# Kernel tuning notes

Measured on AMD Instinct MI355X. Metric: run time of the kernel, lower is better.

The kernel has to match this reference:

```python
import jax, jax.numpy as jnp
import numpy as np

DIM = 512
NUM_HEADS = 8
HEAD_DIM = DIM // NUM_HEADS
EPS = 1e-12  # F.normalize default eps


def _l2norm(x):
    # F.normalize: x / max(||x||_2, eps) along last dim
    n = jnp.sqrt(jnp.sum(x * x, axis=-1, keepdims=True))
    return x / jnp.maximum(n, EPS)


def setup_inputs() -> dict:
    key = jax.random.key(0)
    ks = jax.random.split(key, 7)
    B, N, K = 8, 4096, 256
    scale = 1.0 / np.sqrt(DIM)
    return {
        "X_flat": jax.random.normal(ks[0], (B, N, DIM), jnp.float32),
        "S_tokens": jax.random.normal(ks[1], (B, K, DIM), jnp.float32),
        "Wq": jax.random.normal(ks[2], (DIM, DIM), jnp.float32) * scale,
        "Wk": jax.random.normal(ks[3], (DIM, DIM), jnp.float32) * scale,
        "Wv": jax.random.normal(ks[4], (DIM, DIM), jnp.float32) * scale,
        "Wo": jax.random.normal(ks[5], (DIM, DIM), jnp.float32) * scale,
        "temperature": jnp.ones((NUM_HEADS, 1, 1), jnp.float32),
    }


def reference(X_flat, S_tokens, Wq, Wk, Wv, Wo, temperature):
    B, N, C = X_flat.shape
    K = S_tokens.shape[1]
    H, D = NUM_HEADS, HEAD_DIM
    # torch Linear: y = x @ W.T
    q = (X_flat @ Wq.T).reshape(B, N, H, D).transpose(0, 2, 1, 3)   # (B,H,N,D)
    k = (S_tokens @ Wk.T).reshape(B, K, H, D).transpose(0, 2, 1, 3)  # (B,H,K,D)
    v = (S_tokens @ Wv.T).reshape(B, K, H, D).transpose(0, 2, 1, 3)  # (B,H,K,D)
    q = _l2norm(q)
    k = _l2norm(k)
    attn = jnp.einsum('bhnd,bhkd->bhnk', q, k) * temperature  # temperature (H,1,1) broadcasts
    attn = jax.nn.softmax(attn, axis=-1)
    out = jnp.einsum('bhnk,bhkd->bhnd', attn, v)
    out = out.transpose(0, 2, 1, 3).reshape(B, N, C)
    out = out @ Wo.T
    return X_flat + out
```

## Files before the change

### kernel.cpp

```cpp
#include <hip/hip_runtime.h>
#include <hip/hip_bf16.h>


typedef __bf16 bf16;
typedef __attribute__((ext_vector_type(8))) __bf16 bf16x8;
typedef __attribute__((ext_vector_type(4))) float f32x4;

#if __has_builtin(__builtin_amdgcn_exp2f)
#define EXP2(x) __builtin_amdgcn_exp2f(x)
#else
#define EXP2(x) exp2f(x)
#endif

__device__ __forceinline__ void gload_lds16(const void* g, void* l) {
  __builtin_amdgcn_global_load_lds(
      (__attribute__((address_space(1))) void*)g,
      (__attribute__((address_space(3))) void*)l, 16, 0, 0);
}

__device__ __forceinline__ unsigned pack2(float a, float b) {
  unsigned short x = __builtin_bit_cast(unsigned short, (bf16)a);
  unsigned short y = __builtin_bit_cast(unsigned short, (bf16)b);
  return (unsigned)x | ((unsigned)y << 16);
}

__global__ __launch_bounds__(256) void cvt_all(
    const float* __restrict__ X, const float* __restrict__ S,
    const float* __restrict__ Wq, const float* __restrict__ Wk,
    const float* __restrict__ Wv, const float* __restrict__ Wo,
    bf16* __restrict__ Xb, bf16* __restrict__ Sb, bf16* __restrict__ Wqb,
    bf16* __restrict__ Wkb, bf16* __restrict__ Wvb, bf16* __restrict__ Wob) {
  int i = blockIdx.x * 256 + threadIdx.x;
  const float* src;
  bf16* dst;
  int r;
  if (i < 2097152) {
    src = X; dst = Xb; r = i;
  } else if (i < 2228224) {
    src = S; dst = Sb; r = i - 2097152;
  } else {
    int j = i - 2228224;
    int w = j >> 15;
    r = j & 32767;
    src = (w == 0) ? Wq : (w == 1) ? Wk : (w == 2) ? Wv : Wo;
    dst = (w == 0) ? Wqb : (w == 1) ? Wkb : (w == 2) ? Wvb : Wob;
  }
  float4 a = *(const float4*)(src + (size_t)r * 8);
  float4 b = *(const float4*)(src + (size_t)r * 8 + 4);
  uint4 v;
  v.x = pack2(a.x, a.y);
  v.y = pack2(a.z, a.w);
  v.z = pack2(b.x, b.y);
  v.w = pack2(b.z, b.w);
  *(uint4*)(dst + (size_t)r * 8) = v;
}

__global__ __launch_bounds__(256) void proj_all(
    const bf16* __restrict__ Xb, const bf16* __restrict__ Sb,
    const bf16* __restrict__ Wqb, const bf16* __restrict__ Wkb,
    const bf16* __restrict__ Wvb, const float* __restrict__ temp,
    bf16* __restrict__ Q, bf16* __restrict__ Kn, bf16* __restrict__ Vt) {
  __shared__ __align__(16) char smem[49152];

  const int lg = (blockIdx.x & 7) * 144 + (blockIdx.x >> 3);

  const bf16* A;
  const bf16* W;
  int m0, kind;
  if (lg < 1024) {
    kind = 0; A = Xb; W = Wqb; m0 = (lg >> 2) * 128;
  } else if (lg < 1088) {
    kind = 1; A = Sb; W = Wkb; m0 = ((lg - 1024) >> 2) * 128;
  } else {
    kind = 2; A = Sb; W = Wvb; m0 = ((lg - 1088) >> 2) * 128;
  }
  const int n0 = (lg & 3) * 128;

  const int tid = threadIdx.x;
  const int wid = tid >> 6, lane = tid & 63;
  const int wr = wid >> 1, wc = wid & 1;
  const int g = lane >> 4, c16 = lane & 15;
  const int r0 = tid >> 2, cc0 = tid & 3;
  const int r1 = (256 + tid) >> 2, cc1 = tid & 3;
  const int dst0 = (tid & ~63) * 16, dst1 = (256 + (tid & ~63)) * 16;

  f32x4 acc[4][4] = {};

#define PSTAGE(kb, buf)                                                     \
  {                                                                         \
    char* as = smem + (buf) * 8192;                                         \
    char* bs = smem + 24576 + (buf) * 8192;                                 \
    gload_lds16(A + (size_t)(m0 + r0) * 512 + (kb) + cc0 * 8, as + dst0);   \
    gload_lds16(A + (size_t)(m0 + r1) * 512 + (kb) + cc1 * 8, as + dst1);   \
    gload_lds16(W + (size_t)(n0 + r0) * 512 + (kb) + cc0 * 8, bs + dst0);   \
    gload_lds16(W + (size_t)(n0 + r1) * 512 + (kb) + cc1 * 8, bs + dst1);   \
  }

#define PCOMPUTE(buf)                                                       \
  {                                                                         \
    const bf16* as = (const bf16*)(smem + (buf) * 8192);                    \
    const bf16* bs = (const bf16*)(smem + 24576 + (buf) * 8192);            \
    bf16x8 af[4], bfr[4];                                                   \
    _Pragma("unroll") for (int mi = 0; mi < 4; ++mi) af[mi] =               \
        *(const bf16x8*)(as + (wr * 64 + mi * 16 + c16) * 32 + g * 8);      \
    _Pragma("unroll") for (int ni = 0; ni < 4; ++ni) bfr[ni] =              \
        *(const bf16x8*)(bs + (wc * 64 + ni * 16 + c16) * 32 + g * 8);      \
    _Pragma("unroll") for (int mi = 0; mi < 4; ++mi)                        \
        _Pragma("unroll") for (int ni = 0; ni < 4; ++ni) acc[mi][ni] =      \
            __builtin_amdgcn_mfma_f32_16x16x32_bf16(af[mi], bfr[ni],        \
                                                    acc[mi][ni], 0, 0, 0);  \
  }

  PSTAGE(0, 0);
  PSTAGE(32, 1);
  int bufc = 0;
  for (int t = 0; t < 14; ++t) {
    int bufn = bufc + 2;
    if (bufn >= 3) bufn -= 3;
    PSTAGE((t + 2) * 32, bufn);
    asm volatile("s_waitcnt vmcnt(8)" ::: "memory");
    __builtin_amdgcn_s_barrier();
    PCOMPUTE(bufc);
    __builtin_amdgcn_s_barrier();
    if (++bufc == 3) bufc = 0;
  }
  asm volatile("s_waitcnt vmcnt(4)" ::: "memory");
  __builtin_amdgcn_s_barrier();
  PCOMPUTE(bufc);
  __builtin_amdgcn_s_barrier();
  if (++bufc == 3) bufc = 0;
  asm volatile("s_waitcnt vmcnt(0)" ::: "memory");
  __builtin_amdgcn_s_barrier();
  PCOMPUTE(bufc);

  __syncthreads();

  if (kind != 2) {
    bf16* C = (kind == 0) ? Q : Kn;
    const float sc =
        (kind == 0) ? temp[(n0 + wc * 64) >> 6] * 1.44269504088896f : 1.0f;
    char* eps = smem + wid * 8192;
#pragma unroll
    for (int mi = 0; mi < 4; ++mi) {
      float ss[4];
#pragma unroll
      for (int j = 0; j < 4; ++j) {
        float s = 0.f;
#pragma unroll
        for (int ni = 0; ni < 4; ++ni) {
          float v = acc[mi][ni][j];
          s += v * v;
        }
        ss[j] = s;
      }
#pragma unroll
      for (int msk = 1; msk < 16; msk <<= 1)
#pragma unroll
        for (int j = 0; j < 4; ++j) ss[j] += __shfl_xor(ss[j], msk, 64);
      float inv[4];
#pragma unroll
      for (int j = 0; j < 4; ++j)
        inv[j] = rsqrtf(fmaxf(ss[j], 1e-24f)) * sc;
#pragma unroll
      for (int ni = 0; ni < 4; ++ni)
#pragma unroll
        for (int j = 0; j < 4; ++j) {
          int row = mi * 16 + g * 4 + j, col = ni * 16 + c16;
          int off = (row * 128 + col * 2) ^ ((row & 7) << 4);
          *(bf16*)(eps + off) = (bf16)(acc[mi][ni][j] * inv[j]);
        }
    }
    asm volatile("s_waitcnt lgkmcnt(0)" ::: "memory");
#pragma unroll
    for (int it = 0; it < 8; ++it) {
      int c = it * 64 + lane;
      int row = c >> 3, ch = c & 7;
      int off = (row * 128 + ch * 16) ^ ((row & 7) << 4);
      bf16x8 v = *(const bf16x8*)(eps + off);
      *(bf16x8*)(C + (size_t)(m0 + wr * 64 + row) * 512 + n0 + wc * 64 +
                 ch * 8) = v;
    }
  } else {
#pragma unroll
    for (int mi = 0; mi < 4; ++mi) {
      int m = m0 + wr * 64 + mi * 16 + g * 4;
      int b = m >> 8, tt = m & 255;
#pragma unroll
      for (int ni = 0; ni < 4; ++ni) {
        int col = n0 + wc * 64 + ni * 16 + c16;
        int h = col >> 6, d = col & 63;
        uint2 v;
        v.x = pack2(acc[mi][ni][0], acc[mi][ni][1]);
        v.y = pack2(acc[mi][ni][2], acc[mi][ni][3]);
        *(uint2*)(Vt + ((size_t)((b * 8 + h) * 64 + d) * 256 + tt)) = v;
      }
    }
  }
#undef PSTAGE
#undef PCOMPUTE
}

__global__ __launch_bounds__(256) void out_gemm(
    const bf16* __restrict__ O, const bf16* __restrict__ Wob,
    const float* __restrict__ Xres, float* __restrict__ out) {
  __shared__ __align__(16) char smem[49152];

  const int lg = (blockIdx.x & 7) * 128 + (blockIdx.x >> 3);
  const int m0 = (lg >> 2) * 128, n0 = (lg & 3) * 128;

  const int tid = threadIdx.x;
  const int wid = tid >> 6, lane = tid & 63;
  const int wr = wid >> 1, wc = wid & 1;
  const int g = lane >> 4, c16 = lane & 15;
  const int r0 = tid >> 2, cc0 = tid & 3;
  const int r1 = (256 + tid) >> 2, cc1 = tid & 3;
  const int dst0 = (tid & ~63) * 16, dst1 = (256 + (tid & ~63)) * 16;

  f32x4 acc[4][4] = {};

#define OSTAGE(kb, buf)                                                      \
  {                                                                          \
    char* as = smem + (buf) * 8192;                                          \
    char* bs = smem + 24576 + (buf) * 8192;                                  \
    gload_lds16(O + (size_t)(m0 + r0) * 512 + (kb) + cc0 * 8, as + dst0);    \
    gload_lds16(O + (size_t)(m0 + r1) * 512 + (kb) + cc1 * 8, as + dst1);    \
    gload_lds16(Wob + (size_t)(n0 + r0) * 512 + (kb) + cc0 * 8, bs + dst0);  \
    gload_lds16(Wob + (size_t)(n0 + r1) * 512 + (kb) + cc1 * 8, bs + dst1);  \
  }

#define OCOMPUTE(buf)                                                       \
  {                                                                         \
    const bf16* as = (const bf16*)(smem + (buf) * 8192);                    \
    const bf16* bs = (const bf16*)(smem + 24576 + (buf) * 8192);            \
    bf16x8 af[4], bfr[4];                                                   \
    _Pragma("unroll") for (int mi = 0; mi < 4; ++mi) af[mi] =               \
        *(const bf16x8*)(as + (wr * 64 + mi * 16 + c16) * 32 + g * 8);      \
    _Pragma("unroll") for (int ni = 0; ni < 4; ++ni) bfr[ni] =              \
        *(const bf16x8*)(bs + (wc * 64 + ni * 16 + c16) * 32 + g * 8);      \
    _Pragma("unroll") for (int mi = 0; mi < 4; ++mi)                        \
        _Pragma("unroll") for (int ni = 0; ni < 4; ++ni) acc[mi][ni] =      \
            __builtin_amdgcn_mfma_f32_16x16x32_bf16(af[mi], bfr[ni],        \
                                                    acc[mi][ni], 0, 0, 0);  \
  }

  OSTAGE(0, 0);
  OSTAGE(32, 1);
  int bufc = 0;
  for (int t = 0; t < 14; ++t) {
    int bufn = bufc + 2;
    if (bufn >= 3) bufn -= 3;
    OSTAGE((t + 2) * 32, bufn);
    asm volatile("s_waitcnt vmcnt(8)" ::: "memory");
    __builtin_amdgcn_s_barrier();
    OCOMPUTE(bufc);
    __builtin_amdgcn_s_barrier();
    if (++bufc == 3) bufc = 0;
  }
  asm volatile("s_waitcnt vmcnt(4)" ::: "memory");
  __builtin_amdgcn_s_barrier();
  OCOMPUTE(bufc);
  __builtin_amdgcn_s_barrier();
  if (++bufc == 3) bufc = 0;
  asm volatile("s_waitcnt vmcnt(0)" ::: "memory");
  __builtin_amdgcn_s_barrier();
  OCOMPUTE(bufc);

  __syncthreads();

  char* eps = smem + wid * 8192;
#pragma unroll
  for (int p = 0; p < 2; ++p) {
#pragma unroll
    for (int mm = 0; mm < 2; ++mm)
#pragma unroll
      for (int ni = 0; ni < 4; ++ni)
#pragma unroll
        for (int j = 0; j < 4; ++j) {
          int row = mm * 16 + g * 4 + j, col = ni * 16 + c16;
          int off = (row * 256 + col * 4) ^ ((row & 7) << 4);
          *(float*)(eps + off) = acc[p * 2 + mm][ni][j];
        }
    asm volatile("s_waitcnt lgkmcnt(0)" ::: "memory");
#pragma unroll
    for (int it = 0; it < 8; ++it) {
      int c = it * 64 + lane;
      int row = c >> 4, ch = c & 15;
      int off = (row * 256 + ch * 16) ^ ((row & 7) << 4);
      float4 v = *(const float4*)(eps + off);
      size_t gr = (size_t)(m0 + wr * 64 + p * 32 + row) * 512 + n0 +
                  wc * 64 + ch * 4;
      float4 x = *(const float4*)(Xres + gr);
      v.x += x.x;
      v.y += x.y;
      v.z += x.z;
      v.w += x.w;
      *(float4*)(out + gr) = v;
    }
    asm volatile("s_waitcnt lgkmcnt(0)" ::: "memory");
  }
#undef OSTAGE
#undef OCOMPUTE
}

__global__ __launch_bounds__(256) void attn_fused(
    const bf16* __restrict__ Qn, const bf16* __restrict__ Kn,
    const bf16* __restrict__ Vt, bf16* __restrict__ O) {
  __shared__ __align__(16) char smem[65536];

  const int tid = threadIdx.x;
  const int w = tid >> 6, lane = tid & 63;
  const int g = lane >> 4, c16 = lane & 15;
  const int lg = (blockIdx.x & 7) * 256 + (blockIdx.x >> 3);
  const int nt = lg & 31, h = (lg >> 5) & 7, b = lg >> 8;
  const int n0 = nt * 128;

  {
    const bf16* Ksrc = Kn + ((size_t)b * 256) * 512 + h * 64;
    const bf16* Vsrc = Vt + (size_t)((b * 8 + h) * 64) * 256;
#pragma unroll
    for (int it = 0; it < 8; ++it) {
      int base = it * 256 + w * 64;
      int c = base + lane;
      int ii = c >> 6, rr = c & 63;
      int fc16 = rr >> 2, fg = rr & 3;
      int kmi = ii >> 1, ks_ = ii & 1;
      gload_lds16(Ksrc + (size_t)(kmi * 16 + fc16) * 512 + ks_ * 32 + fg * 8,
                  smem + base * 16);
      int vks = ii >> 2, vni = ii & 3;
      gload_lds16(Vsrc + (size_t)(vni * 16 + fc16) * 256 + vks * 32 + fg * 8,
                  smem + 32768 + base * 16);
    }
  }
  const bf16* Qsrc = Qn + ((size_t)b * 4096 + n0) * 512 + h * 64;
  bf16x8 qf0[2], qf1[2];
  {
    const bf16* q0 = Qsrc + (size_t)(w * 16 + c16) * 512;
    const bf16* q1 = Qsrc + (size_t)(64 + w * 16 + c16) * 512;
    qf0[0] = *(const bf16x8*)(q0 + g * 8);
    qf0[1] = *(const bf16x8*)(q0 + 32 + g * 8);
    qf1[0] = *(const bf16x8*)(q1 + g * 8);
    qf1[1] = *(const bf16x8*)(q1 + 32 + g * 8);
  }
  __syncthreads();

  f32x4 sacc0[16] = {}, sacc1[16] = {};
#pragma unroll
  for (int mi = 0; mi < 16; ++mi) {
#pragma unroll
    for (int s = 0; s < 2; ++s) {
      bf16x8 kf =
          *(const bf16x8*)(smem + ((mi * 2 + s) * 64 + c16 * 4 + g) * 16);
      sacc0[mi] = __builtin_amdgcn_mfma_f32_16x16x32_bf16(kf, qf0[s],
                                                          sacc0[mi], 0, 0, 0);
      sacc1[mi] = __builtin_amdgcn_mfma_f32_16x16x32_bf16(kf, qf1[s],
                                                          sacc1[mi], 0, 0, 0);
    }
  }

  float mxa[4] = {-1e30f, -1e30f, -1e30f, -1e30f};
  float mxb[4] = {-1e30f, -1e30f, -1e30f, -1e30f};
#pragma unroll
  for (int mi = 0; mi < 16; ++mi)
#pragma unroll
    for (int j = 0; j < 4; ++j) {
      mxa[j] = fmaxf(mxa[j], sacc0[mi][j]);
      mxb[j] = fmaxf(mxb[j], sacc1[mi][j]);
    }
  float mx0 = fmaxf(fmaxf(mxa[0], mxa[1]), fmaxf(mxa[2], mxa[3]));
  float mx1 = fmaxf(fmaxf(mxb[0], mxb[1]), fmaxf(mxb[2], mxb[3]));
  mx0 = fmaxf(mx0, __shfl_xor(mx0, 16, 64));
  mx0 = fmaxf(mx0, __shfl_xor(mx0, 32, 64));
  mx1 = fmaxf(mx1, __shfl_xor(mx1, 16, 64));
  mx1 = fmaxf(mx1, __shfl_xor(mx1, 32, 64));
  float sa[4] = {0.f, 0.f, 0.f, 0.f}, sb[4] = {0.f, 0.f, 0.f, 0.f};
#pragma unroll
  for (int mi = 0; mi < 16; ++mi)
#pragma unroll
    for (int j = 0; j < 4; ++j) {
      float p0 = EXP2(sacc0[mi][j] - mx0);
      float p1 = EXP2(sacc1[mi][j] - mx1);
      sacc0[mi][j] = p0;
      sacc1[mi][j] = p1;
      sa[j] += p0;
      sb[j] += p1;
    }
  float sum0 = (sa[0] + sa[1]) + (sa[2] + sa[3]);
  float sum1 = (sb[0] + sb[1]) + (sb[2] + sb[3]);
  sum0 += __shfl_xor(sum0, 16, 64);
  sum0 += __shfl_xor(sum0, 32, 64);
  sum1 += __shfl_xor(sum1, 16, 64);
  sum1 += __shfl_xor(sum1, 32, 64);
  float inv0 = 1.0f / sum0, inv1 = 1.0f / sum1;

  __syncthreads();

  char* pslice = smem + w * 8192;

#define DO_PV(SACC, INV, P)                                                  \
  {                                                                          \
    _Pragma("unroll") for (int mi = 0; mi < 16; ++mi) {                      \
      int cl = (mi >> 1) * 64 + c16 * 4 + ((mi & 1) * 2 + (g >> 1));         \
      uint2 v;                                                               \
      v.x = pack2(SACC[mi][0], SACC[mi][1]);                                 \
      v.y = pack2(SACC[mi][2], SACC[mi][3]);                                 \
      *(uint2*)(pslice + cl * 16 + (g & 1) * 8) = v;                         \
    }                                                                        \
    asm volatile("s_waitcnt lgkmcnt(0)" ::: "memory");                       \
    __builtin_amdgcn_sched_barrier(0);                                       \
    f32x4 oacc[4] = {};                                                      \
    _Pragma("unroll") for (int ks = 0; ks < 8; ++ks) {                       \
      bf16x8 pa =                                                            \
          *(const bf16x8*)(pslice + (ks * 64 + c16 * 4 + g) * 16);           \
      _Pragma("unroll") for (int ni = 0; ni < 4; ++ni) {                     \
        bf16x8 vb = *(const bf16x8*)(                                        \
            smem + 32768 + ((ks * 4 + ni) * 64 + c16 * 4 + g) * 16);         \
        oacc[ni] = __builtin_amdgcn_mfma_f32_16x16x32_bf16(pa, vb,           \
                                                           oacc[ni], 0,0,0); \
      }                                                                      \
    }                                                                        \
    asm volatile("s_waitcnt lgkmcnt(0)" ::: "memory");                       \
    __builtin_amdgcn_sched_barrier(0);                                       \
    _Pragma("unroll") for (int ni = 0; ni < 4; ++ni)                         \
        _Pragma("unroll") for (int j = 0; j < 4; ++j) {                      \
      int row = g * 4 + j, col = ni * 16 + c16;                              \
      int off = (row * 128 + col * 2) ^ ((row & 7) << 4);                    \
      *(bf16*)(pslice + off) = (bf16)(oacc[ni][j] * (INV));                  \
    }                                                                        \
    asm volatile("s_waitcnt lgkmcnt(0)" ::: "memory");                       \
    __builtin_amdgcn_sched_barrier(0);                                       \
    _Pragma("unroll") for (int it = 0; it < 2; ++it) {                       \
      int c = it * 64 + lane;                                                \
      int row = c >> 3, ch = c & 7;                                          \
      int off = (row * 128 + ch * 16) ^ ((row & 7) << 4);                    \
      bf16x8 v = *(const bf16x8*)(pslice + off);                             \
      *(bf16x8*)(O + ((size_t)b * 4096 + n0 + (P) * 64 + w * 16 + row) *     \
                         512 + h * 64 + ch * 8) = v;                         \
    }                                                                        \
    asm volatile("s_waitcnt lgkmcnt(0)" ::: "memory");                       \
    __builtin_amdgcn_sched_barrier(0);                                       \
  }

  DO_PV(sacc0, inv0, 0);
  DO_PV(sacc1, inv1, 1);
#undef DO_PV
}

extern "C" void kernel_launch(void* const* d_in, const int* in_sizes, int n_in,
                              void* d_out, int out_size, void* d_ws,
                              size_t ws_size, hipStream_t stream) {
  const float* X = (const float*)d_in[0];
  const float* S = (const float*)d_in[1];
  const float* Wq = (const float*)d_in[2];
  const float* Wk = (const float*)d_in[3];
  const float* Wv = (const float*)d_in[4];
  const float* Wo = (const float*)d_in[5];
  const float* temp = (const float*)d_in[6];
  float* out = (float*)d_out;

  char* ws = (char*)d_ws;
  bf16* Qws = (bf16*)ws;
  bf16* Kws = (bf16*)(ws + 33554432);
  bf16* Vtws = (bf16*)(ws + 35651584);
  bf16* Wqb = (bf16*)(ws + 37748736);
  bf16* Wkb = (bf16*)(ws + 38273024);
  bf16* Wvb = (bf16*)(ws + 38797312);
  bf16* Wob = (bf16*)(ws + 39321600);

  bf16* Xb = (bf16*)d_out;
  bf16* Sb = (bf16*)((char*)d_out + 33554432);

  cvt_all<<<dim3(9216), dim3(256), 0, stream>>>(X, S, Wq, Wk, Wv, Wo, Xb, Sb,
                                                Wqb, Wkb, Wvb, Wob);
  proj_all<<<dim3(1152), dim3(256), 0, stream>>>(Xb, Sb, Wqb, Wkb, Wvb, temp,
                                                 Qws, Kws, Vtws);
  attn_fused<<<dim3(2048), dim3(256), 0, stream>>>(Qws, Kws, Vtws, Qws);
  out_gemm<<<dim3(1024), dim3(256), 0, stream>>>(Qws, Wob, X, out);
}
```

Before: 148.3 us.

## Store Q/K/V in MFMA-fragment order so attention loads are contiguous

The projection epilogue now writes Q, K and V directly in the per-(batch,head) fragment order that the attention MFMAs consume. Attention can then load K/V into LDS and Q into registers with contiguous per-lane 16-byte accesses instead of strided row gathers. The projection is split into two launches, K/V first and then Q, because Q now reuses the bf16 S buffer region in the output and must be written after S is consumed. This adds a launch and scattered epilogue stores in exchange for simpler, coalesced loads in the attention kernel.

```diff
diff --git a/kernel.cpp b/kernel.cpp
--- a/kernel.cpp
+++ b/kernel.cpp
@@ -55,26 +55,34 @@
   *(uint4*)(dst + (size_t)r * 8) = v;
 }
 
+template <int PHASE>
 __global__ __launch_bounds__(256) void proj_all(
     const bf16* __restrict__ Xb, const bf16* __restrict__ Sb,
     const bf16* __restrict__ Wqb, const bf16* __restrict__ Wkb,
     const bf16* __restrict__ Wvb, const float* __restrict__ temp,
-    bf16* __restrict__ Q, bf16* __restrict__ Kn, bf16* __restrict__ Vt) {
+    bf16* __restrict__ Qf, bf16* __restrict__ Kf, bf16* __restrict__ Vf) {
   __shared__ __align__(16) char smem[49152];
-
-  const int lg = (blockIdx.x & 7) * 144 + (blockIdx.x >> 3);
 
   const bf16* A;
   const bf16* W;
-  int m0, kind;
-  if (lg < 1024) {
-    kind = 0; A = Xb; W = Wqb; m0 = (lg >> 2) * 128;
-  } else if (lg < 1088) {
-    kind = 1; A = Sb; W = Wkb; m0 = ((lg - 1024) >> 2) * 128;
+  int m0, n0, kind;
+  if (PHASE == 0) {
+    const int lg = (blockIdx.x & 7) * 128 + (blockIdx.x >> 3);
+    kind = 0; A = Xb; W = Wqb;
+    m0 = (lg >> 2) * 128;
+    n0 = (lg & 3) * 128;
   } else {
-    kind = 2; A = Sb; W = Wvb; m0 = ((lg - 1088) >> 2) * 128;
-  }
-  const int n0 = (lg & 3) * 128;
+    const int lg = (blockIdx.x & 7) * 16 + (blockIdx.x >> 3);
+    if (lg < 64) {
+      kind = 1; A = Sb; W = Wkb;
+      m0 = (lg >> 2) * 128;
+      n0 = (lg & 3) * 128;
+    } else {
+      kind = 2; A = Sb; W = Wvb;
+      m0 = ((lg - 64) >> 2) * 128;
+      n0 = ((lg - 64) & 3) * 128;
+    }
+  }
 
   const int tid = threadIdx.x;
   const int wid = tid >> 6, lane = tid & 63;
@@ -136,7 +144,6 @@
   __syncthreads();
 
   if (kind != 2) {
-    bf16* C = (kind == 0) ? Q : Kn;
     const float sc =
         (kind == 0) ? temp[(n0 + wc * 64) >> 6] * 1.44269504088896f : 1.0f;
     char* eps = smem + wid * 8192;
@@ -171,28 +178,44 @@
         }
     }
     asm volatile("s_waitcnt lgkmcnt(0)" ::: "memory");
+    __builtin_amdgcn_sched_barrier(0);
 #pragma unroll
     for (int it = 0; it < 8; ++it) {
       int c = it * 64 + lane;
       int row = c >> 3, ch = c & 7;
       int off = (row * 128 + ch * 16) ^ ((row & 7) << 4);
       bf16x8 v = *(const bf16x8*)(eps + off);
-      *(bf16x8*)(C + (size_t)(m0 + wr * 64 + row) * 512 + n0 + wc * 64 +
-                 ch * 8) = v;
+      int rg = m0 + wr * 64 + row;
+      int cg = n0 + wc * 64 + ch * 8;
+      int hh = cg >> 6, d0 = cg & 63;
+      if (kind == 0) {
+        int bb = rg >> 12, qr = rg & 4095;
+        int unit = ((qr >> 4) * 2 + (d0 >> 5)) * 64 + ((d0 & 31) >> 3) * 16 +
+                   (qr & 15);
+        *(bf16x8*)(Qf + (((size_t)(bb * 8 + hh)) << 18) + unit * 8) = v;
+      } else {
+        int bb = rg >> 8, tt = rg & 255;
+        int unit = ((tt >> 4) * 2 + (d0 >> 5)) * 64 + ((d0 & 31) >> 3) * 16 +
+                   (tt & 15);
+        *(bf16x8*)(Kf + (((size_t)(bb * 8 + hh)) << 14) + unit * 8) = v;
+      }
     }
   } else {
 #pragma unroll
     for (int mi = 0; mi < 4; ++mi) {
       int m = m0 + wr * 64 + mi * 16 + g * 4;
-      int b = m >> 8, tt = m & 255;
+      int bb = m >> 8, tt = m & 255;
 #pragma unroll
       for (int ni = 0; ni < 4; ++ni) {
         int col = n0 + wc * 64 + ni * 16 + c16;
-        int h = col >> 6, d = col & 63;
+        int hh = col >> 6, d = col & 63;
+        int unit = ((tt >> 5) * 4 + (d >> 4)) * 64 + ((tt >> 3) & 3) * 16 +
+                   (d & 15);
         uint2 v;
         v.x = pack2(acc[mi][ni][0], acc[mi][ni][1]);
         v.y = pack2(acc[mi][ni][2], acc[mi][ni][3]);
-        *(uint2*)(Vt + ((size_t)((b * 8 + h) * 64 + d) * 256 + tt)) = v;
+        *(uint2*)(Vf + (((size_t)(bb * 8 + hh)) << 14) + unit * 8 +
+                  (tt & 7)) = v;
       }
     }
   }
@@ -281,6 +304,7 @@
           *(float*)(eps + off) = acc[p * 2 + mm][ni][j];
         }
     asm volatile("s_waitcnt lgkmcnt(0)" ::: "memory");
+    __builtin_amdgcn_sched_barrier(0);
 #pragma unroll
     for (int it = 0; it < 8; ++it) {
       int c = it * 64 + lane;
@@ -297,14 +321,15 @@
       *(float4*)(out + gr) = v;
     }
     asm volatile("s_waitcnt lgkmcnt(0)" ::: "memory");
+    __builtin_amdgcn_sched_barrier(0);
   }
 #undef OSTAGE
 #undef OCOMPUTE
 }
 
 __global__ __launch_bounds__(256) void attn_fused(
-    const bf16* __restrict__ Qn, const bf16* __restrict__ Kn,
-    const bf16* __restrict__ Vt, bf16* __restrict__ O) {
+    const bf16* __restrict__ Qf, const bf16* __restrict__ Kf,
+    const bf16* __restrict__ Vf, bf16* __restrict__ O) {
   __shared__ __align__(16) char smem[65536];
 
   const int tid = threadIdx.x;
@@ -314,32 +339,24 @@
   const int nt = lg & 31, h = (lg >> 5) & 7, b = lg >> 8;
   const int n0 = nt * 128;
 
-  {
-    const bf16* Ksrc = Kn + ((size_t)b * 256) * 512 + h * 64;
-    const bf16* Vsrc = Vt + (size_t)((b * 8 + h) * 64) * 256;
-#pragma unroll
-    for (int it = 0; it < 8; ++it) {
-      int base = it * 256 + w * 64;
-      int c = base + lane;
-      int ii = c >> 6, rr = c & 63;
-      int fc16 = rr >> 2, fg = rr & 3;
-      int kmi = ii >> 1, ks_ = ii & 1;
-      gload_lds16(Ksrc + (size_t)(kmi * 16 + fc16) * 512 + ks_ * 32 + fg * 8,
-                  smem + base * 16);
-      int vks = ii >> 2, vni = ii & 3;
-      gload_lds16(Vsrc + (size_t)(vni * 16 + fc16) * 256 + vks * 32 + fg * 8,
-                  smem + 32768 + base * 16);
-    }
-  }
-  const bf16* Qsrc = Qn + ((size_t)b * 4096 + n0) * 512 + h * 64;
+  const bf16* Kimg = Kf + (((size_t)(b * 8 + h)) << 14);
+  const bf16* Vimg = Vf + (((size_t)(b * 8 + h)) << 14);
+  const bf16* Qimg = Qf + (((size_t)(b * 8 + h)) << 18);
+
+#pragma unroll
+  for (int it = 0; it < 8; ++it) {
+    int base = it * 256 + w * 64;
+    gload_lds16(Kimg + (size_t)(base + lane) * 8, smem + base * 16);
+    gload_lds16(Vimg + (size_t)(base + lane) * 8, smem + 32768 + base * 16);
+  }
   bf16x8 qf0[2], qf1[2];
   {
-    const bf16* q0 = Qsrc + (size_t)(w * 16 + c16) * 512;
-    const bf16* q1 = Qsrc + (size_t)(64 + w * 16 + c16) * 512;
-    qf0[0] = *(const bf16x8*)(q0 + g * 8);
-    qf0[1] = *(const bf16x8*)(q0 + 32 + g * 8);
-    qf1[0] = *(const bf16x8*)(q1 + g * 8);
-    qf1[1] = *(const bf16x8*)(q1 + 32 + g * 8);
+    int u0 = (nt * 8 + w) * 2;
+    int u1 = (nt * 8 + 4 + w) * 2;
+    qf0[0] = *(const bf16x8*)(Qimg + (size_t)((u0 + 0) * 64 + lane) * 8);
+    qf0[1] = *(const bf16x8*)(Qimg + (size_t)((u0 + 1) * 64 + lane) * 8);
+    qf1[0] = *(const bf16x8*)(Qimg + (size_t)((u1 + 0) * 64 + lane) * 8);
+    qf1[1] = *(const bf16x8*)(Qimg + (size_t)((u1 + 1) * 64 + lane) * 8);
   }
   __syncthreads();
 
@@ -348,8 +365,7 @@
   for (int mi = 0; mi < 16; ++mi) {
 #pragma unroll
     for (int s = 0; s < 2; ++s) {
-      bf16x8 kf =
-          *(const bf16x8*)(smem + ((mi * 2 + s) * 64 + c16 * 4 + g) * 16);
+      bf16x8 kf = *(const bf16x8*)(smem + ((mi * 2 + s) * 64 + lane) * 16);
       sacc0[mi] = __builtin_amdgcn_mfma_f32_16x16x32_bf16(kf, qf0[s],
                                                           sacc0[mi], 0, 0, 0);
       sacc1[mi] = __builtin_amdgcn_mfma_f32_16x16x32_bf16(kf, qf1[s],
@@ -399,21 +415,20 @@
 #define DO_PV(SACC, INV, P)                                                  \
   {                                                                          \
     _Pragma("unroll") for (int mi = 0; mi < 16; ++mi) {                      \
-      int cl = (mi >> 1) * 64 + c16 * 4 + ((mi & 1) * 2 + (g >> 1));         \
+      int un = (mi >> 1) * 64 + ((mi & 1) * 2 + (g >> 1)) * 16 + c16;        \
       uint2 v;                                                               \
       v.x = pack2(SACC[mi][0], SACC[mi][1]);                                 \
       v.y = pack2(SACC[mi][2], SACC[mi][3]);                                 \
-      *(uint2*)(pslice + cl * 16 + (g & 1) * 8) = v;                         \
+      *(uint2*)(pslice + un * 16 + (g & 1) * 8) = v;                         \
     }                                                                        \
     asm volatile("s_waitcnt lgkmcnt(0)" ::: "memory");                       \
     __builtin_amdgcn_sched_barrier(0);                                       \
     f32x4 oacc[4] = {};                                                      \
     _Pragma("unroll") for (int ks = 0; ks < 8; ++ks) {                       \
-      bf16x8 pa =                                                            \
-          *(const bf16x8*)(pslice + (ks * 64 + c16 * 4 + g) * 16);           \
+      bf16x8 pa = *(const bf16x8*)(pslice + (ks * 64 + lane) * 16);          \
       _Pragma("unroll") for (int ni = 0; ni < 4; ++ni) {                     \
-        bf16x8 vb = *(const bf16x8*)(                                        \
-            smem + 32768 + ((ks * 4 + ni) * 64 + c16 * 4 + g) * 16);         \
+        bf16x8 vb = *(const bf16x8*)(smem + 32768 +                          \
+                                     ((ks * 4 + ni) * 64 + lane) * 16);      \
         oacc[ni] = __builtin_amdgcn_mfma_f32_16x16x32_bf16(pa, vb,           \
                                                            oacc[ni], 0,0,0); \
       }                                                                      \
@@ -458,9 +473,9 @@
   float* out = (float*)d_out;
 
   char* ws = (char*)d_ws;
-  bf16* Qws = (bf16*)ws;
-  bf16* Kws = (bf16*)(ws + 33554432);
-  bf16* Vtws = (bf16*)(ws + 35651584);
+  bf16* Ows = (bf16*)ws;
+  bf16* Kf = (bf16*)(ws + 33554432);
+  bf16* Vf = (bf16*)(ws + 35651584);
   bf16* Wqb = (bf16*)(ws + 37748736);
   bf16* Wkb = (bf16*)(ws + 38273024);
   bf16* Wvb = (bf16*)(ws + 38797312);
@@ -468,11 +483,14 @@
 
   bf16* Xb = (bf16*)d_out;
   bf16* Sb = (bf16*)((char*)d_out + 33554432);
+  bf16* Qf = (bf16*)((char*)d_out + 33554432);
 
   cvt_all<<<dim3(9216), dim3(256), 0, stream>>>(X, S, Wq, Wk, Wv, Wo, Xb, Sb,
                                                 Wqb, Wkb, Wvb, Wob);
-  proj_all<<<dim3(1152), dim3(256), 0, stream>>>(Xb, Sb, Wqb, Wkb, Wvb, temp,
-                                                 Qws, Kws, Vtws);
-  attn_fused<<<dim3(2048), dim3(256), 0, stream>>>(Qws, Kws, Vtws, Qws);
-  out_gemm<<<dim3(1024), dim3(256), 0, stream>>>(Qws, Wob, X, out);
-}
+  proj_all<1><<<dim3(128), dim3(256), 0, stream>>>(Xb, Sb, Wqb, Wkb, Wvb,
+                                                   temp, Qf, Kf, Vf);
+  proj_all<0><<<dim3(1024), dim3(256), 0, stream>>>(Xb, Sb, Wqb, Wkb, Wvb,
+                                                    temp, Qf, Kf, Vf);
+  attn_fused<<<dim3(2048), dim3(256), 0, stream>>>(Qf, Kf, Vf, Ows);
+  out_gemm<<<dim3(1024), dim3(256), 0, stream>>>(Ows, Wob, X, out);
+}
```

Result: faster. 141.6 us (-4.5%).
